# Kernel optimization log

Measured on AMD Instinct MI355X. Metric: run time of the kernel, lower is better.

## Reference

```python
import jax, jax.numpy as jnp
import numpy as np

N_CHANNELS = 29
HIDDEN = [5, 4, 4]
IN_FEAT = 7
OUT_FEAT = 3
EPS = 1e-07


def _glorot(key, fan_in, fan_out, shape):
    lim = np.sqrt(6.0 / (fan_in + fan_out))
    return jax.random.uniform(key, shape, jnp.float32, -lim, lim)


def _make_params(key):
    # Batched per-channel weights: stack n_channels tiny MLPs along leading dim.
    sizes = [IN_FEAT] + HIDDEN + [OUT_FEAT]
    Ws, bs = [], []
    for i in range(len(sizes) - 1):
        key, k = jax.random.split(key)
        Ws.append(_glorot(k, sizes[i], sizes[i + 1], (N_CHANNELS, sizes[i], sizes[i + 1])))
        bs.append(jnp.zeros((N_CHANNELS, sizes[i + 1]), jnp.float32))
    return Ws, bs


def setup_inputs() -> dict:
    key = jax.random.key(0)
    ks = jax.random.split(key, 16)
    N = 262144
    inp = {
        "tau": jax.random.uniform(ks[0], (N, N_CHANNELS, 1), jnp.float32),
        "mu": jax.random.uniform(ks[1], (N, 1), jnp.float32, 0.05, 1.0),
        "mu_bar": jax.random.uniform(ks[2], (N, 1), jnp.float32, 0.05, 1.0),
        "lw": jax.random.uniform(ks[3], (N, 1), jnp.float32),
        "h2o": jax.random.uniform(ks[4], (N, 1), jnp.float32),
        "o3": jax.random.uniform(ks[5], (N, 1), jnp.float32),
        "co2": jax.random.uniform(ks[6], (N, 1), jnp.float32),
        "u": jax.random.uniform(ks[7], (N, 1), jnp.float32),
        "n2o": jax.random.uniform(ks[8], (N, 1), jnp.float32),
        "ch4": jax.random.uniform(ks[9], (N, 1), jnp.float32),
    }
    Wd, bd = _make_params(ks[10])
    Wf, bf = _make_params(ks[11])
    for i in range(4):
        inp[f"Wd{i}"] = Wd[i]
        inp[f"bd{i}"] = bd[i]
        inp[f"Wf{i}"] = Wf[i]
        inp[f"bf{i}"] = bf[i]
    return inp


def _mlp(x, Ws, bs):
    # x: [N, F]; Ws[i]: [C, fin, fout]; output [N, C, 3]
    h = jnp.einsum('nf,cfh->nch', x, Ws[0]) + bs[0]
    h = jax.nn.relu(h)
    for i in (1, 2):
        h = jnp.einsum('nch,chk->nck', h, Ws[i]) + bs[i]
        h = jax.nn.relu(h)
    h = jnp.einsum('nch,chk->nck', h, Ws[3]) + bs[3]
    return jax.nn.softmax(h, axis=-1)


def reference(tau, mu, mu_bar, lw, h2o, o3, co2, u, n2o, ch4,
              Wd0, bd0, Wd1, bd1, Wd2, bd2, Wd3, bd3,
              Wf0, bf0, Wf1, bf1, Wf2, bf2, Wf3, bf3):
    constituents = jnp.concatenate([lw, h2o, o3, co2, u, n2o, ch4], axis=1)  # [N,7]
    c_direct = constituents / (mu + EPS)
    c_diffuse = constituents / (mu_bar + EPS)
    mu3 = mu[:, :, None]          # [N,1,1]
    mu_bar3 = mu_bar[:, :, None]
    tau_total = jnp.sum(tau, axis=-1, keepdims=True)  # [N,C,1]
    t_direct = jnp.exp(-tau_total / (mu3 + EPS))       # [N,C,1]
    t_diffuse = jnp.exp(-tau_total / (mu_bar3 + EPS))
    e_direct = _mlp(c_direct, [Wd0, Wd1, Wd2, Wd3], [bd0, bd1, bd2, bd3])    # [N,C,3]
    e_diffuse = _mlp(c_diffuse, [Wf0, Wf1, Wf2, Wf3], [bf0, bf1, bf2, bf3])  # [N,C,3]
    return jnp.concatenate([t_direct, t_diffuse, e_direct, e_diffuse], axis=2)  # [N,C,8]
```

## Files before the change

kernel.cpp:

```cpp
#include <hip/hip_runtime.h>

#define EPS 1e-7f
#define NCH 29
#define SPB 128
#define ROWF4 17


typedef float f32x2 __attribute__((ext_vector_type(2)));

__device__ __forceinline__ f32x2 splat2(float v) { f32x2 r; r.x = v; r.y = v; return r; }
__device__ __forceinline__ f32x2 fma2(f32x2 a, f32x2 b, f32x2 c) {
    return __builtin_elementwise_fma(a, b, c);
}
__device__ __forceinline__ f32x2 max2(f32x2 a, f32x2 b) {
    return __builtin_elementwise_max(a, b);
}
__device__ __forceinline__ f32x2 expc2(f32x2 a) {
    f32x2 r; r.x = __expf(a.x); r.y = __expf(a.y); return r;
}
__device__ __forceinline__ f32x2 rcp2(f32x2 a) {
    f32x2 r; r.x = __builtin_amdgcn_rcpf(a.x); r.y = __builtin_amdgcn_rcpf(a.y); return r;
}

__device__ __forceinline__ void mlp7p(const f32x2 x[7],
    const float* __restrict__ W0, const float* __restrict__ b0,
    const float* __restrict__ W1, const float* __restrict__ b1,
    const float* __restrict__ W2, const float* __restrict__ b2,
    const float* __restrict__ W3, const float* __restrict__ b3,
    f32x2 e[3])
{
    const f32x2 zero = splat2(0.0f);
    f32x2 h0[5];
#pragma unroll
    for (int h = 0; h < 5; ++h) {
        f32x2 a = splat2(b0[h]);
#pragma unroll
        for (int f = 0; f < 7; ++f) a = fma2(x[f], splat2(W0[f * 5 + h]), a);
        h0[h] = max2(a, zero);
    }
    f32x2 h1[4];
#pragma unroll
    for (int k = 0; k < 4; ++k) {
        f32x2 a = splat2(b1[k]);
#pragma unroll
        for (int h = 0; h < 5; ++h) a = fma2(h0[h], splat2(W1[h * 4 + k]), a);
        h1[k] = max2(a, zero);
    }
    f32x2 h2[4];
#pragma unroll
    for (int k = 0; k < 4; ++k) {
        f32x2 a = splat2(b2[k]);
#pragma unroll
        for (int h = 0; h < 4; ++h) a = fma2(h1[h], splat2(W2[h * 4 + k]), a);
        h2[k] = max2(a, zero);
    }
    f32x2 l[3];
#pragma unroll
    for (int k = 0; k < 3; ++k) {
        f32x2 a = splat2(b3[k]);
#pragma unroll
        for (int h = 0; h < 4; ++h) a = fma2(h2[h], splat2(W3[h * 3 + k]), a);
        l[k] = a;
    }
    f32x2 m = max2(l[0], max2(l[1], l[2]));
    f32x2 e0 = expc2(l[0] - m);
    f32x2 e1 = expc2(l[1] - m);
    f32x2 e2 = expc2(l[2] - m);
    f32x2 rs = rcp2(e0 + e1 + e2);
    e[0] = e0 * rs; e[1] = e1 * rs; e[2] = e2 * rs;
}

__global__ __launch_bounds__(256, 4) void lps_kernel(
    const float* __restrict__ tau, const float* __restrict__ mu, const float* __restrict__ mu_bar,
    const float* __restrict__ lw, const float* __restrict__ h2o, const float* __restrict__ o3,
    const float* __restrict__ co2, const float* __restrict__ uu, const float* __restrict__ n2o,
    const float* __restrict__ ch4,
    const float* __restrict__ Wd0, const float* __restrict__ bd0,
    const float* __restrict__ Wf0, const float* __restrict__ bf0,
    const float* __restrict__ Wd1, const float* __restrict__ bd1,
    const float* __restrict__ Wf1, const float* __restrict__ bf1,
    const float* __restrict__ Wd2, const float* __restrict__ bd2,
    const float* __restrict__ Wf2, const float* __restrict__ bf2,
    const float* __restrict__ Wd3, const float* __restrict__ bd3,
    const float* __restrict__ Wf3, const float* __restrict__ bf3,
    float* __restrict__ out, int N)
{
    __shared__ __align__(16) float4 obuf[SPB * ROWF4];

    const int tid  = threadIdx.x;
    const int lane = tid & 63;
    const int wid  = __builtin_amdgcn_readfirstlane(tid >> 6);

    const int base = blockIdx.x * SPB;
    const int s0 = base + lane;
    const int s1 = s0 + 64;
    const int i0 = (s0 < N) ? s0 : (N - 1);
    const int i1 = (s1 < N) ? s1 : (N - 1);

    f32x2 mu2, mub2;
    mu2.x  = mu[i0];      mu2.y  = mu[i1];
    mub2.x = mu_bar[i0];  mub2.y = mu_bar[i1];
    const f32x2 rmu2  = rcp2(mu2 + splat2(EPS));
    const f32x2 rmub2 = rcp2(mub2 + splat2(EPS));
    const f32x2 nrmu2  = -rmu2;
    const f32x2 nrmub2 = -rmub2;

    f32x2 cons2[7];
    cons2[0].x = lw[i0];  cons2[0].y = lw[i1];
    cons2[1].x = h2o[i0]; cons2[1].y = h2o[i1];
    cons2[2].x = o3[i0];  cons2[2].y = o3[i1];
    cons2[3].x = co2[i0]; cons2[3].y = co2[i1];
    cons2[4].x = uu[i0];  cons2[4].y = uu[i1];
    cons2[5].x = n2o[i0]; cons2[5].y = n2o[i1];
    cons2[6].x = ch4[i0]; cons2[6].y = ch4[i1];

    f32x2 x2d[7], x2f[7];
#pragma unroll
    for (int f = 0; f < 7; ++f) { x2d[f] = cons2[f] * rmu2; x2f[f] = cons2[f] * rmub2; }

    int nsamp = N - base;
    if (nsamp > SPB) nsamp = SPB;
    float4* out4 = (float4*)out;

#pragma unroll
    for (int p = 0; p < 4; ++p) {
        const int cbase = p * 8;
        const int cend  = (p == 3) ? NCH : (cbase + 8);

        for (int c = cbase + wid; c < cend; c += 4) {
            f32x2 tau2;
            tau2.x = tau[(size_t)i0 * NCH + c];
            tau2.y = tau[(size_t)i1 * NCH + c];
            f32x2 td2 = expc2(tau2 * nrmu2);
            f32x2 tf2 = expc2(tau2 * nrmub2);

            f32x2 ed[3], ef[3];
            mlp7p(x2d, Wd0 + c * 35, bd0 + c * 5, Wd1 + c * 20, bd1 + c * 4,
                       Wd2 + c * 16, bd2 + c * 4, Wd3 + c * 12, bd3 + c * 3, ed);
            mlp7p(x2f, Wf0 + c * 35, bf0 + c * 5, Wf1 + c * 20, bf1 + c * 4,
                       Wf2 + c * 16, bf2 + c * 4, Wf3 + c * 12, bf3 + c * 3, ef);

            const int r = (c - cbase) * 2;
            obuf[lane * ROWF4 + r]            = make_float4(td2.x, tf2.x, ed[0].x, ed[1].x);
            obuf[lane * ROWF4 + r + 1]        = make_float4(ed[2].x, ef[0].x, ef[1].x, ef[2].x);
            obuf[(lane + 64) * ROWF4 + r]     = make_float4(td2.y, tf2.y, ed[0].y, ed[1].y);
            obuf[(lane + 64) * ROWF4 + r + 1] = make_float4(ed[2].y, ef[0].y, ef[1].y, ef[2].y);
        }
        __syncthreads();

        if (p < 3) {
            const int tot = nsamp * 16;
            for (int i = tid; i < tot; i += 256) {
                const int s = i >> 4, r = i & 15;
                out4[(size_t)(base + s) * 58 + p * 16 + r] = obuf[s * ROWF4 + r];
            }
        } else {
            const int tot = nsamp * 10;
            for (int i = tid; i < tot; i += 256) {
                const int s = i / 10, r = i - s * 10;
                out4[(size_t)(base + s) * 58 + 48 + r] = obuf[s * ROWF4 + r];
            }
        }
        __syncthreads();
    }
}

extern "C" void kernel_launch(void* const* d_in, const int* in_sizes, int n_in,
                              void* d_out, int out_size, void* d_ws, size_t ws_size,
                              hipStream_t stream) {
    const float* tau    = (const float*)d_in[0];
    const float* mu     = (const float*)d_in[1];
    const float* mu_bar = (const float*)d_in[2];
    const float* lw     = (const float*)d_in[3];
    const float* h2o    = (const float*)d_in[4];
    const float* o3     = (const float*)d_in[5];
    const float* co2    = (const float*)d_in[6];
    const float* uu     = (const float*)d_in[7];
    const float* n2o    = (const float*)d_in[8];
    const float* ch4    = (const float*)d_in[9];

    const float* Wd0 = (const float*)d_in[10];
    const float* bd0 = (const float*)d_in[11];
    const float* Wf0 = (const float*)d_in[12];
    const float* bf0 = (const float*)d_in[13];
    const float* Wd1 = (const float*)d_in[14];
    const float* bd1 = (const float*)d_in[15];
    const float* Wf1 = (const float*)d_in[16];
    const float* bf1 = (const float*)d_in[17];
    const float* Wd2 = (const float*)d_in[18];
    const float* bd2 = (const float*)d_in[19];
    const float* Wf2 = (const float*)d_in[20];
    const float* bf2 = (const float*)d_in[21];
    const float* Wd3 = (const float*)d_in[22];
    const float* bd3 = (const float*)d_in[23];
    const float* Wf3 = (const float*)d_in[24];
    const float* bf3 = (const float*)d_in[25];

    float* out = (float*)d_out;
    int N = in_sizes[1];

    int blocks = (N + SPB - 1) / SPB;
    lps_kernel<<<blocks, 256, 0, stream>>>(
        tau, mu, mu_bar, lw, h2o, o3, co2, uu, n2o, ch4,
        Wd0, bd0, Wf0, bf0, Wd1, bd1, Wf1, bf1,
        Wd2, bd2, Wf2, bf2, Wd3, bd3, Wf3, bf3,
        out, N);
}
```

Baseline: 83.91 us.

## Use 512-thread blocks and stage full sample rows for contiguous output stores

Doubles the block to 8 wavefronts, so each wave handles about 4 channels in one pass instead of looping over 4 channel groups with a sync after each. The shared buffer now holds all 58 float4s for 64 samples, so each half-block's output is written as one fully contiguous run rather than 16-float4 fragments per sample. The second sample's results wait in registers until the first half is written, which raises register pressure. The stride-58 row loop also needs a division by 58.

```diff
diff --git a/kernel.cpp b/kernel.cpp
--- a/kernel.cpp
+++ b/kernel.cpp
@@ -3,7 +3,7 @@
 #define EPS 1e-7f
 #define NCH 29
 #define SPB 128
-#define ROWF4 17
+#define ROWF4 59
 
 
 typedef float f32x2 __attribute__((ext_vector_type(2)));
@@ -70,7 +70,7 @@
     e[0] = e0 * rs; e[1] = e1 * rs; e[2] = e2 * rs;
 }
 
-__global__ __launch_bounds__(256, 4) void lps_kernel(
+__global__ __launch_bounds__(512, 4) void lps_kernel(
     const float* __restrict__ tau, const float* __restrict__ mu, const float* __restrict__ mu_bar,
     const float* __restrict__ lw, const float* __restrict__ h2o, const float* __restrict__ o3,
     const float* __restrict__ co2, const float* __restrict__ uu, const float* __restrict__ n2o,
@@ -85,14 +85,14 @@
     const float* __restrict__ Wf3, const float* __restrict__ bf3,
     float* __restrict__ out, int N)
 {
-    __shared__ __align__(16) float4 obuf[SPB * ROWF4];
+    __shared__ __align__(16) float4 obuf[64 * ROWF4];
 
     const int tid  = threadIdx.x;
     const int lane = tid & 63;
     const int wid  = __builtin_amdgcn_readfirstlane(tid >> 6);
 
-    const int base = blockIdx.x * SPB;
-    const int s0 = base + lane;
+    const long long base = (long long)blockIdx.x * SPB;
+    const int s0 = (int)base + lane;
     const int s1 = s0 + 64;
     const int i0 = (s0 < N) ? s0 : (N - 1);
     const int i1 = (s1 < N) ? s1 : (N - 1);
@@ -100,8 +100,8 @@
     f32x2 mu2, mub2;
     mu2.x  = mu[i0];      mu2.y  = mu[i1];
     mub2.x = mu_bar[i0];  mub2.y = mu_bar[i1];
-    const f32x2 rmu2  = rcp2(mu2 + splat2(EPS));
-    const f32x2 rmub2 = rcp2(mub2 + splat2(EPS));
+    const f32x2 rmu2   = rcp2(mu2 + splat2(EPS));
+    const f32x2 rmub2  = rcp2(mub2 + splat2(EPS));
     const f32x2 nrmu2  = -rmu2;
     const f32x2 nrmub2 = -rmub2;
 
@@ -118,16 +118,12 @@
 #pragma unroll
     for (int f = 0; f < 7; ++f) { x2d[f] = cons2[f] * rmu2; x2f[f] = cons2[f] * rmub2; }
 
-    int nsamp = N - base;
-    if (nsamp > SPB) nsamp = SPB;
-    float4* out4 = (float4*)out;
-
-#pragma unroll
-    for (int p = 0; p < 4; ++p) {
-        const int cbase = p * 8;
-        const int cend  = (p == 3) ? NCH : (cbase + 8);
-
-        for (int c = cbase + wid; c < cend; c += 4) {
+    float ry[4][8];
+
+#pragma unroll
+    for (int it = 0; it < 4; ++it) {
+        const int c = wid + it * 8;
+        if (c < NCH) {
             f32x2 tau2;
             tau2.x = tau[(size_t)i0 * NCH + c];
             tau2.y = tau[(size_t)i1 * NCH + c];
@@ -140,28 +136,51 @@
             mlp7p(x2f, Wf0 + c * 35, bf0 + c * 5, Wf1 + c * 20, bf1 + c * 4,
                        Wf2 + c * 16, bf2 + c * 4, Wf3 + c * 12, bf3 + c * 3, ef);
 
-            const int r = (c - cbase) * 2;
-            obuf[lane * ROWF4 + r]            = make_float4(td2.x, tf2.x, ed[0].x, ed[1].x);
-            obuf[lane * ROWF4 + r + 1]        = make_float4(ed[2].x, ef[0].x, ef[1].x, ef[2].x);
-            obuf[(lane + 64) * ROWF4 + r]     = make_float4(td2.y, tf2.y, ed[0].y, ed[1].y);
-            obuf[(lane + 64) * ROWF4 + r + 1] = make_float4(ed[2].y, ef[0].y, ef[1].y, ef[2].y);
-        }
-        __syncthreads();
-
-        if (p < 3) {
-            const int tot = nsamp * 16;
-            for (int i = tid; i < tot; i += 256) {
-                const int s = i >> 4, r = i & 15;
-                out4[(size_t)(base + s) * 58 + p * 16 + r] = obuf[s * ROWF4 + r];
+            obuf[lane * ROWF4 + c * 2]     = make_float4(td2.x, tf2.x, ed[0].x, ed[1].x);
+            obuf[lane * ROWF4 + c * 2 + 1] = make_float4(ed[2].x, ef[0].x, ef[1].x, ef[2].x);
+            ry[it][0] = td2.y;   ry[it][1] = tf2.y;
+            ry[it][2] = ed[0].y; ry[it][3] = ed[1].y;
+            ry[it][4] = ed[2].y; ry[it][5] = ef[0].y;
+            ry[it][6] = ef[1].y; ry[it][7] = ef[2].y;
+        }
+    }
+
+    float4* out4 = (float4*)out;
+
+    __syncthreads();
+    {
+        int n0 = N - (int)base; n0 = (n0 > 64) ? 64 : n0;
+        if (n0 > 0) {
+            const int tot = n0 * 58;
+            const long long ob = base * 58;
+            for (int i = tid; i < tot; i += 512) {
+                const int s = i / 58, r = i - s * 58;
+                out4[ob + i] = obuf[s * ROWF4 + r];
             }
-        } else {
-            const int tot = nsamp * 10;
-            for (int i = tid; i < tot; i += 256) {
-                const int s = i / 10, r = i - s * 10;
-                out4[(size_t)(base + s) * 58 + 48 + r] = obuf[s * ROWF4 + r];
+        }
+    }
+    __syncthreads();
+
+#pragma unroll
+    for (int it = 0; it < 4; ++it) {
+        const int c = wid + it * 8;
+        if (c < NCH) {
+            obuf[lane * ROWF4 + c * 2]     = make_float4(ry[it][0], ry[it][1], ry[it][2], ry[it][3]);
+            obuf[lane * ROWF4 + c * 2 + 1] = make_float4(ry[it][4], ry[it][5], ry[it][6], ry[it][7]);
+        }
+    }
+    __syncthreads();
+
+    {
+        int n1 = N - (int)base - 64; n1 = (n1 > 64) ? 64 : n1;
+        if (n1 > 0) {
+            const int tot = n1 * 58;
+            const long long ob = (base + 64) * 58;
+            for (int i = tid; i < tot; i += 512) {
+                const int s = i / 58, r = i - s * 58;
+                out4[ob + i] = obuf[s * ROWF4 + r];
             }
         }
-        __syncthreads();
     }
 }
 
@@ -200,7 +219,7 @@
     int N = in_sizes[1];
 
     int blocks = (N + SPB - 1) / SPB;
-    lps_kernel<<<blocks, 256, 0, stream>>>(
+    lps_kernel<<<blocks, 512, 0, stream>>>(
         tau, mu, mu_bar, lw, h2o, o3, co2, uu, n2o, ch4,
         Wd0, bd0, Wf0, bf0, Wd1, bd1, Wf1, bf1,
         Wd2, bd2, Wf2, bf2, Wd3, bd3, Wf3, bf3,
```

Result: no change. 83.54 us (-0.4%).
